# Kernel optimization log

Hardware: AMD Instinct MI355X
Metric: run time of the kernel (lower is better)

Reference implementation:

```python
import jax, jax.numpy as jnp
import numpy as np

WINDOW = 128
LOOK_BACKWARD = 1
LOOK_FORWARD = 0
PAD_VALUE = -1


def look_around(x, backward=LOOK_BACKWARD, forward=LOOK_FORWARD, pad_value=PAD_VALUE):
    # x: [b, windows, window_size, ...]; pad along windows axis, concat along window_size axis
    pad_width = [(0, 0)] * x.ndim
    pad_width[1] = (backward, forward)
    px = jnp.pad(x, pad_width, constant_values=pad_value)
    w = x.shape[1]
    return jnp.concatenate([px[:, i:i + w] for i in range(forward + backward + 1)], axis=2)


def rotate_half(x):
    x1, x2 = jnp.split(x, 2, axis=-1)
    return jnp.concatenate([-x2, x1], axis=-1)


def setup_inputs() -> dict:
    key = jax.random.key(0)
    k1, k2, k3 = jax.random.split(key, 3)
    B, H, N, D = 4, 16, 4096, 64
    return {
        "q": jax.random.normal(k1, (B, H, N, D), dtype=jnp.float32),
        "k": jax.random.normal(k2, (B, H, N, D), dtype=jnp.float32),
        "v": jax.random.normal(k3, (B, H, N, D), dtype=jnp.float32),
    }


def reference(q, k, v):
    B, H, N, D = q.shape
    qf = q.reshape(B * H, N, D)
    kf = k.reshape(B * H, N, D)
    vf = v.reshape(B * H, N, D)

    # --- inline rotary (SinusoidalEmbeddings + apply_rotary_pos_emb) ---
    inv_freq = 1.0 / (10000.0 ** (jnp.arange(0, D, 2, dtype=jnp.float32) / D))  # [D/2]
    t = jnp.arange(N, dtype=jnp.float32)
    half = t[:, None] * inv_freq[None, :]                      # [N, D/2]
    freqs = jnp.concatenate([half, half], axis=-1)             # [N, D]
    cos, sin = jnp.cos(freqs), jnp.sin(freqs)
    qf = qf * cos + rotate_half(qf) * sin
    kf = kf * cos + rotate_half(kf) * sin

    # --- blocked local attention ---
    w = WINDOW
    windows = N // w
    scale = D ** -0.5
    bq = qf.reshape(B * H, windows, w, D)
    bk = look_around(kf.reshape(B * H, windows, w, D))         # [bh, windows, j, D]
    bv = look_around(vf.reshape(B * H, windows, w, D))

    seq = jnp.arange(N).reshape(1, windows, w)
    bq_t = seq[..., :, None]                                   # [1, windows, w, 1]
    bq_k = look_around(seq)[..., None, :]                      # [1, windows, 1, j]

    sim = jnp.einsum('bwie,bwje->bwij', bq, bk) * scale        # [bh, windows, w, j]
    mask_value = -jnp.finfo(sim.dtype).max
    sim = jnp.where(bq_t < bq_k, mask_value, sim)              # causal mask

    attn = jax.nn.softmax(sim, axis=-1)
    out = jnp.einsum('bwij,bwje->bwie', attn, bv)              # [bh, windows, w, D]
    return out.reshape(B, H, N, D)
```

## Files before the change

### kernel.cpp

```cpp
#include <hip/hip_runtime.h>
#include <hip/hip_bf16.h>

typedef __attribute__((ext_vector_type(8))) short  short8;
typedef __attribute__((ext_vector_type(4))) short  short4v;
typedef __attribute__((ext_vector_type(4))) float  float4v;

#define MFMA_QK(A,B,C) __builtin_amdgcn_mfma_f32_16x16x32_bf16(A,B,C,0,0,0)
#define MFMA_PV(A,B,C) __builtin_amdgcn_mfma_f32_16x16x16bf16_1k(A,B,C,0,0,0)

static __device__ __forceinline__ short f2bf(float x) {
  unsigned u = __float_as_uint(x);
  u += 0x7fffu + ((u >> 16) & 1u);
  return (short)(u >> 16);
}

static __device__ __forceinline__ void rope_sc(float rev, float& sn, float& cs) {
  float fr = rev - floorf(rev);
  sn = __builtin_amdgcn_sinf(fr);
  cs = __builtin_amdgcn_cosf(fr);
}

static __device__ __forceinline__ float invfreq_rev(int idx) {
  return exp2f(-0.41524101186092034f * (float)idx) * 0.15915494309189535f;
}

#define N_ 4096
#define D_ 64
#define W_ 128

__global__ __launch_bounds__(256, 2)
void la_fused(const float* __restrict__ qg, const float* __restrict__ kg,
              const float* __restrict__ vg, float* __restrict__ outg)
{
  __shared__ __attribute__((aligned(16))) short Kl[256][72];
  __shared__ __attribute__((aligned(16))) short Vl[64][264];

  const int blk  = blockIdx.x;
  const int w    = blk & 31;
  const int bh   = blk >> 5;
  const int base = bh * (N_ * D_);
  const int tid  = threadIdx.x;

  {
    const float* kb = kg + base;
    const float* vb = vg + base;
#pragma unroll
    for (int it = 0; it < 8; ++it) {
      int tau = it * 256 + tid;
      int j   = tau >> 3;
      int d0  = (tau & 7) << 2;
      int g   = w * W_ - W_ + j;
      float klo[4], khi[4], vlo[4], vhi[4];
      if (g < 0) {
#pragma unroll
        for (int dd = 0; dd < 4; ++dd) { klo[dd]=khi[dd]=vlo[dd]=vhi[dd] = -1.0f; }
      } else {
        float4v a   = *(const float4v*)(kb + g * D_ + d0);
        float4v b   = *(const float4v*)(kb + g * D_ + d0 + 32);
        float4v va  = *(const float4v*)(vb + g * D_ + d0);
        float4v vb2 = *(const float4v*)(vb + g * D_ + d0 + 32);
        const float t = (float)g;
#pragma unroll
        for (int dd = 0; dd < 4; ++dd) {
          float sn, cs; rope_sc(t * invfreq_rev(d0 + dd), sn, cs);
          klo[dd] = a[dd] * cs - b[dd] * sn;
          khi[dd] = b[dd] * cs + a[dd] * sn;
          vlo[dd] = va[dd]; vhi[dd] = vb2[dd];
        }
      }
      short4v k0 = { f2bf(klo[0]), f2bf(klo[1]), f2bf(klo[2]), f2bf(klo[3]) };
      short4v k1 = { f2bf(khi[0]), f2bf(khi[1]), f2bf(khi[2]), f2bf(khi[3]) };
      *(short4v*)&Kl[j][d0]      = k0;
      *(short4v*)&Kl[j][d0 + 32] = k1;
#pragma unroll
      for (int dd = 0; dd < 4; ++dd) {
        Vl[d0 + dd][j]      = f2bf(vlo[dd]);
        Vl[d0 + 32 + dd][j] = f2bf(vhi[dd]);
      }
    }
  }
  __syncthreads();

  const int lane = tid & 63;
  const int wv   = tid >> 6;
  const int il   = lane & 15;
  const int qd   = lane >> 4;

  short8 qf[2][2];
#pragma unroll
  for (int ii = 0; ii < 2; ++ii) {
    const int rw = wv * 32 + ii * 16 + il;
    const int n  = w * W_ + rw;
    const float* qr = qg + base + n * D_ + qd * 8;
    float4v x0 = *(const float4v*)(qr);
    float4v x1 = *(const float4v*)(qr + 4);
    float4v y0 = *(const float4v*)(qr + 32);
    float4v y1 = *(const float4v*)(qr + 36);
    float lo[8], hi[8];
    const float t = (float)n;
#pragma unroll
    for (int jj = 0; jj < 8; ++jj) {
      const int d = qd * 8 + jj;
      float xx = (jj < 4) ? x0[jj & 3] : x1[jj & 3];
      float yy = (jj < 4) ? y0[jj & 3] : y1[jj & 3];
      float sn, cs; rope_sc(t * invfreq_rev(d), sn, cs);
      lo[jj] = xx * cs - yy * sn;
      hi[jj] = yy * cs + xx * sn;
    }
    qf[ii][0] = short8{ f2bf(lo[0]),f2bf(lo[1]),f2bf(lo[2]),f2bf(lo[3]),
                        f2bf(lo[4]),f2bf(lo[5]),f2bf(lo[6]),f2bf(lo[7]) };
    qf[ii][1] = short8{ f2bf(hi[0]),f2bf(hi[1]),f2bf(hi[2]),f2bf(hi[3]),
                        f2bf(hi[4]),f2bf(hi[5]),f2bf(hi[6]),f2bf(hi[7]) };
  }

  float4v S[2][16];
#pragma unroll
  for (int ii = 0; ii < 2; ++ii)
#pragma unroll
    for (int t = 0; t < 16; ++t) { float4v z = {0.f,0.f,0.f,0.f}; S[ii][t] = z; }

#pragma unroll
  for (int t = 0; t < 16; ++t) {
    short8 a0 = *(const short8*)&Kl[t * 16 + il][qd * 8];
    short8 a1 = *(const short8*)&Kl[t * 16 + il][32 + qd * 8];
#pragma unroll
    for (int ii = 0; ii < 2; ++ii) {
      S[ii][t] = MFMA_QK(a0, qf[ii][0], S[ii][t]);
      S[ii][t] = MFMA_QK(a1, qf[ii][1], S[ii][t]);
    }
  }

  short4v P[2][16];
  float   invsum[2];
#pragma unroll
  for (int ii = 0; ii < 2; ++ii) {
    const int rw = wv * 32 + ii * 16 + il;
    float mx = -3.0e38f;
#pragma unroll
    for (int t = 0; t < 16; ++t) {
#pragma unroll
      for (int r = 0; r < 4; ++r) {
        const int j = t * 16 + qd * 4 + r;
        float s = S[ii][t][r] * 0.125f;
        if (j > rw + 128) s = -3.0e38f;
        S[ii][t][r] = s;
        mx = fmaxf(mx, s);
      }
    }
    mx = fmaxf(mx, __shfl_xor(mx, 16));
    mx = fmaxf(mx, __shfl_xor(mx, 32));
    float sum = 0.0f;
#pragma unroll
    for (int t = 0; t < 16; ++t) {
#pragma unroll
      for (int r = 0; r < 4; ++r) {
        float p = __expf(S[ii][t][r] - mx);
        S[ii][t][r] = p;
        sum += p;
      }
    }
    sum += __shfl_xor(sum, 16);
    sum += __shfl_xor(sum, 32);
    invsum[ii] = 1.0f / sum;
#pragma unroll
    for (int t = 0; t < 16; ++t) {
      P[ii][t] = short4v{ f2bf(S[ii][t][0]), f2bf(S[ii][t][1]),
                          f2bf(S[ii][t][2]), f2bf(S[ii][t][3]) };
    }
  }

  float4v O[2][4];
#pragma unroll
  for (int ii = 0; ii < 2; ++ii)
#pragma unroll
    for (int dt = 0; dt < 4; ++dt) { float4v z = {0.f,0.f,0.f,0.f}; O[ii][dt] = z; }

#pragma unroll
  for (int c = 0; c < 16; ++c) {
    short4v af[4];
#pragma unroll
    for (int dt = 0; dt < 4; ++dt)
      af[dt] = *(const short4v*)&Vl[dt * 16 + il][c * 16 + qd * 4];
#pragma unroll
    for (int dt = 0; dt < 4; ++dt) {
      O[0][dt] = MFMA_PV(af[dt], P[0][c], O[0][dt]);
      O[1][dt] = MFMA_PV(af[dt], P[1][c], O[1][dt]);
    }
  }

#pragma unroll
  for (int ii = 0; ii < 2; ++ii) {
    const int n = w * W_ + wv * 32 + ii * 16 + il;
    float* op = outg + base + n * D_;
    const float inv = invsum[ii];
#pragma unroll
    for (int dt = 0; dt < 4; ++dt) {
      float4v o = O[ii][dt];
      o[0] *= inv; o[1] *= inv; o[2] *= inv; o[3] *= inv;
      *(float4v*)(op + dt * 16 + qd * 4) = o;
    }
  }
}

extern "C" void kernel_launch(void* const* d_in, const int* in_sizes, int n_in,
                              void* d_out, int out_size, void* d_ws, size_t ws_size,
                              hipStream_t stream)
{
  const float* q = (const float*)d_in[0];
  const float* k = (const float*)d_in[1];
  const float* v = (const float*)d_in[2];
  float* out = (float*)d_out;
  la_fused<<<dim3(64 * 32), dim3(256), 0, stream>>>(q, k, v, out);
}
```

Baseline: 226.1 us.

## Precompute rotary table, repack V layout, fold scale into Q, cheaper bf16 packing

Adds a small kernel that writes cos/sin tables to the workspace so the main kernel loads rotary factors instead of evaluating sin/cos per element. V is stored in shared memory in a chunked [j/4][d][4] layout with vectorized stores, replacing scalar transposed writes. The softmax scale and log2(e) are folded into Q so softmax uses exp2 and rcp. The mask is only evaluated on tiles that may be masked, and bf16 conversion uses round-half-up with a byte permute. Trade-offs are an extra launch, extra memory traffic for the table reads, and slightly different rounding.

```diff
diff --git a/kernel.cpp b/kernel.cpp
--- a/kernel.cpp
+++ b/kernel.cpp
@@ -1,17 +1,24 @@
 #include <hip/hip_runtime.h>
 #include <hip/hip_bf16.h>
 
-typedef __attribute__((ext_vector_type(8))) short  short8;
-typedef __attribute__((ext_vector_type(4))) short  short4v;
-typedef __attribute__((ext_vector_type(4))) float  float4v;
+typedef __attribute__((ext_vector_type(8))) short    short8;
+typedef __attribute__((ext_vector_type(4))) short    short4v;
+typedef __attribute__((ext_vector_type(4))) float    float4v;
+typedef __attribute__((ext_vector_type(2))) unsigned uint2v;
+typedef __attribute__((ext_vector_type(4))) unsigned uint4v;
 
 #define MFMA_QK(A,B,C) __builtin_amdgcn_mfma_f32_16x16x32_bf16(A,B,C,0,0,0)
 #define MFMA_PV(A,B,C) __builtin_amdgcn_mfma_f32_16x16x16bf16_1k(A,B,C,0,0,0)
 
-static __device__ __forceinline__ short f2bf(float x) {
-  unsigned u = __float_as_uint(x);
-  u += 0x7fffu + ((u >> 16) & 1u);
-  return (short)(u >> 16);
+#define N_ 4096
+#define D_ 64
+#define W_ 128
+#define QSCALE 0.18033688011112042f
+
+static __device__ __forceinline__ unsigned pk2(float a, float b) {
+  unsigned ua = __float_as_uint(a) + 0x8000u;
+  unsigned ub = __float_as_uint(b) + 0x8000u;
+  return __builtin_amdgcn_perm(ub, ua, 0x07060302u);
 }
 
 static __device__ __forceinline__ void rope_sc(float rev, float& sn, float& cs) {
@@ -19,99 +26,148 @@
   sn = __builtin_amdgcn_sinf(fr);
   cs = __builtin_amdgcn_cosf(fr);
 }
-
 static __device__ __forceinline__ float invfreq_rev(int idx) {
   return exp2f(-0.41524101186092034f * (float)idx) * 0.15915494309189535f;
 }
 
-#define N_ 4096
-#define D_ 64
-#define W_ 128
-
+__global__ void gen_tab(float* __restrict__ cosT, float* __restrict__ sinT) {
+  int i = blockIdx.x * 256 + threadIdx.x;
+  int n = i >> 5, d = i & 31;
+  float sn, cs;
+  rope_sc((float)n * invfreq_rev(d), sn, cs);
+  cosT[i] = cs; sinT[i] = sn;
+}
+
+template<bool TAB>
 __global__ __launch_bounds__(256, 2)
 void la_fused(const float* __restrict__ qg, const float* __restrict__ kg,
-              const float* __restrict__ vg, float* __restrict__ outg)
+              const float* __restrict__ vg, float* __restrict__ outg,
+              const float* __restrict__ cosT, const float* __restrict__ sinT)
 {
   __shared__ __attribute__((aligned(16))) short Kl[256][72];
-  __shared__ __attribute__((aligned(16))) short Vl[64][264];
+  __shared__ __attribute__((aligned(16))) short Vt[64][68][4];
 
   const int blk  = blockIdx.x;
   const int w    = blk & 31;
   const int bh   = blk >> 5;
   const int base = bh * (N_ * D_);
   const int tid  = threadIdx.x;
+  const int lane = tid & 63;
+  const int wv   = tid >> 6;
+  const int il   = lane & 15;
+  const int qd   = lane >> 4;
 
   {
     const float* kb = kg + base;
-    const float* vb = vg + base;
 #pragma unroll
     for (int it = 0; it < 8; ++it) {
       int tau = it * 256 + tid;
       int j   = tau >> 3;
       int d0  = (tau & 7) << 2;
       int g   = w * W_ - W_ + j;
-      float klo[4], khi[4], vlo[4], vhi[4];
+      uint2v w0, w1;
       if (g < 0) {
-#pragma unroll
-        for (int dd = 0; dd < 4; ++dd) { klo[dd]=khi[dd]=vlo[dd]=vhi[dd] = -1.0f; }
+        unsigned m1 = pk2(-1.0f, -1.0f);
+        w0 = uint2v{m1, m1}; w1 = w0;
       } else {
-        float4v a   = *(const float4v*)(kb + g * D_ + d0);
-        float4v b   = *(const float4v*)(kb + g * D_ + d0 + 32);
-        float4v va  = *(const float4v*)(vb + g * D_ + d0);
-        float4v vb2 = *(const float4v*)(vb + g * D_ + d0 + 32);
-        const float t = (float)g;
+        float4v a = *(const float4v*)(kb + g * D_ + d0);
+        float4v b = *(const float4v*)(kb + g * D_ + d0 + 32);
+        float4v cs, sn;
+        if constexpr (TAB) {
+          cs = *(const float4v*)(cosT + g * 32 + d0);
+          sn = *(const float4v*)(sinT + g * 32 + d0);
+        } else {
+          const float t = (float)g;
+#pragma unroll
+          for (int dd = 0; dd < 4; ++dd) { float s_, c_; rope_sc(t * invfreq_rev(d0 + dd), s_, c_); sn[dd]=s_; cs[dd]=c_; }
+        }
+        float lo[4], hi[4];
 #pragma unroll
         for (int dd = 0; dd < 4; ++dd) {
-          float sn, cs; rope_sc(t * invfreq_rev(d0 + dd), sn, cs);
-          klo[dd] = a[dd] * cs - b[dd] * sn;
-          khi[dd] = b[dd] * cs + a[dd] * sn;
-          vlo[dd] = va[dd]; vhi[dd] = vb2[dd];
+          lo[dd] = a[dd] * cs[dd] - b[dd] * sn[dd];
+          hi[dd] = b[dd] * cs[dd] + a[dd] * sn[dd];
         }
-      }
-      short4v k0 = { f2bf(klo[0]), f2bf(klo[1]), f2bf(klo[2]), f2bf(klo[3]) };
-      short4v k1 = { f2bf(khi[0]), f2bf(khi[1]), f2bf(khi[2]), f2bf(khi[3]) };
-      *(short4v*)&Kl[j][d0]      = k0;
-      *(short4v*)&Kl[j][d0 + 32] = k1;
+        w0 = uint2v{ pk2(lo[0], lo[1]), pk2(lo[2], lo[3]) };
+        w1 = uint2v{ pk2(hi[0], hi[1]), pk2(hi[2], hi[3]) };
+      }
+      *(uint2v*)&Kl[j][d0]      = w0;
+      *(uint2v*)&Kl[j][d0 + 32] = w1;
+    }
+  }
+
+  {
+    const float* vb = vg + base;
+    const int m  = tid & 15;
+    const int d0 = m << 2;
+#pragma unroll
+    for (int pv = 0; pv < 4; ++pv) {
+      int j0 = ((tid >> 4) + pv * 16) << 2;
+      int g0 = w * W_ - W_ + j0;
+      float vv[4][4];
+      if (g0 < 0) {
+#pragma unroll
+        for (int rr = 0; rr < 4; ++rr)
+#pragma unroll
+          for (int cc = 0; cc < 4; ++cc) vv[rr][cc] = -1.0f;
+      } else {
+#pragma unroll
+        for (int rr = 0; rr < 4; ++rr) {
+          float4v r = *(const float4v*)(vb + (g0 + rr) * D_ + d0);
+          vv[rr][0]=r[0]; vv[rr][1]=r[1]; vv[rr][2]=r[2]; vv[rr][3]=r[3];
+        }
+      }
+      const int chunk = j0 >> 2;
 #pragma unroll
       for (int dd = 0; dd < 4; ++dd) {
-        Vl[d0 + dd][j]      = f2bf(vlo[dd]);
-        Vl[d0 + 32 + dd][j] = f2bf(vhi[dd]);
-      }
-    }
-  }
-  __syncthreads();
-
-  const int lane = tid & 63;
-  const int wv   = tid >> 6;
-  const int il   = lane & 15;
-  const int qd   = lane >> 4;
+        int cc = (dd + m) & 3;
+        uint2v wvv = uint2v{ pk2(vv[0][cc], vv[1][cc]), pk2(vv[2][cc], vv[3][cc]) };
+        *(uint2v*)&Vt[chunk][d0 + cc][0] = wvv;
+      }
+    }
+  }
 
   short8 qf[2][2];
 #pragma unroll
   for (int ii = 0; ii < 2; ++ii) {
-    const int rw = wv * 32 + ii * 16 + il;
-    const int n  = w * W_ + rw;
+    const int n = w * W_ + wv * 32 + ii * 16 + il;
     const float* qr = qg + base + n * D_ + qd * 8;
     float4v x0 = *(const float4v*)(qr);
     float4v x1 = *(const float4v*)(qr + 4);
     float4v y0 = *(const float4v*)(qr + 32);
     float4v y1 = *(const float4v*)(qr + 36);
+    float4v c0, c1, s0, s1;
+    if constexpr (TAB) {
+      c0 = *(const float4v*)(cosT + n * 32 + qd * 8);
+      c1 = *(const float4v*)(cosT + n * 32 + qd * 8 + 4);
+      s0 = *(const float4v*)(sinT + n * 32 + qd * 8);
+      s1 = *(const float4v*)(sinT + n * 32 + qd * 8 + 4);
+    } else {
+      const float t = (float)n;
+#pragma unroll
+      for (int dd = 0; dd < 4; ++dd) {
+        float s_, c_;
+        rope_sc(t * invfreq_rev(qd * 8 + dd), s_, c_);     s0[dd]=s_; c0[dd]=c_;
+        rope_sc(t * invfreq_rev(qd * 8 + 4 + dd), s_, c_); s1[dd]=s_; c1[dd]=c_;
+      }
+    }
     float lo[8], hi[8];
-    const float t = (float)n;
 #pragma unroll
     for (int jj = 0; jj < 8; ++jj) {
-      const int d = qd * 8 + jj;
       float xx = (jj < 4) ? x0[jj & 3] : x1[jj & 3];
       float yy = (jj < 4) ? y0[jj & 3] : y1[jj & 3];
-      float sn, cs; rope_sc(t * invfreq_rev(d), sn, cs);
-      lo[jj] = xx * cs - yy * sn;
-      hi[jj] = yy * cs + xx * sn;
-    }
-    qf[ii][0] = short8{ f2bf(lo[0]),f2bf(lo[1]),f2bf(lo[2]),f2bf(lo[3]),
-                        f2bf(lo[4]),f2bf(lo[5]),f2bf(lo[6]),f2bf(lo[7]) };
-    qf[ii][1] = short8{ f2bf(hi[0]),f2bf(hi[1]),f2bf(hi[2]),f2bf(hi[3]),
-                        f2bf(hi[4]),f2bf(hi[5]),f2bf(hi[6]),f2bf(hi[7]) };
-  }
+      float cs = (jj < 4) ? c0[jj & 3] : c1[jj & 3];
+      float sn = (jj < 4) ? s0[jj & 3] : s1[jj & 3];
+      float xs = xx * QSCALE, ys = yy * QSCALE;
+      lo[jj] = xs * cs - ys * sn;
+      hi[jj] = ys * cs + xs * sn;
+    }
+    uint4v pa = uint4v{ pk2(lo[0],lo[1]), pk2(lo[2],lo[3]), pk2(lo[4],lo[5]), pk2(lo[6],lo[7]) };
+    uint4v pb = uint4v{ pk2(hi[0],hi[1]), pk2(hi[2],hi[3]), pk2(hi[4],hi[5]), pk2(hi[6],hi[7]) };
+    qf[ii][0] = __builtin_bit_cast(short8, pa);
+    qf[ii][1] = __builtin_bit_cast(short8, pb);
+  }
+
+  __syncthreads();
 
   float4v S[2][16];
 #pragma unroll
@@ -134,15 +190,16 @@
   float   invsum[2];
 #pragma unroll
   for (int ii = 0; ii < 2; ++ii) {
-    const int rw = wv * 32 + ii * 16 + il;
-    float mx = -3.0e38f;
+    const int rw   = wv * 32 + ii * 16 + il;
+    const int jcap = rw + 128;
+    float mx = -1.0e30f;
 #pragma unroll
     for (int t = 0; t < 16; ++t) {
+      bool maybe = (t * 16 + 15) > (wv * 32 + ii * 16 + 128);
 #pragma unroll
       for (int r = 0; r < 4; ++r) {
-        const int j = t * 16 + qd * 4 + r;
-        float s = S[ii][t][r] * 0.125f;
-        if (j > rw + 128) s = -3.0e38f;
+        float s = S[ii][t][r];
+        if (maybe) { int j = t * 16 + qd * 4 + r; if (j > jcap) s = -1.0e30f; }
         S[ii][t][r] = s;
         mx = fmaxf(mx, s);
       }
@@ -151,21 +208,20 @@
     mx = fmaxf(mx, __shfl_xor(mx, 32));
     float sum = 0.0f;
 #pragma unroll
-    for (int t = 0; t < 16; ++t) {
+    for (int t = 0; t < 16; ++t)
 #pragma unroll
       for (int r = 0; r < 4; ++r) {
-        float p = __expf(S[ii][t][r] - mx);
+        float p = __builtin_amdgcn_exp2f(S[ii][t][r] - mx);
         S[ii][t][r] = p;
         sum += p;
       }
-    }
     sum += __shfl_xor(sum, 16);
     sum += __shfl_xor(sum, 32);
-    invsum[ii] = 1.0f / sum;
+    invsum[ii] = __builtin_amdgcn_rcpf(sum);
 #pragma unroll
     for (int t = 0; t < 16; ++t) {
-      P[ii][t] = short4v{ f2bf(S[ii][t][0]), f2bf(S[ii][t][1]),
-                          f2bf(S[ii][t][2]), f2bf(S[ii][t][3]) };
+      uint2v pw = uint2v{ pk2(S[ii][t][0], S[ii][t][1]), pk2(S[ii][t][2], S[ii][t][3]) };
+      P[ii][t] = __builtin_bit_cast(short4v, pw);
     }
   }
 
@@ -180,7 +236,7 @@
     short4v af[4];
 #pragma unroll
     for (int dt = 0; dt < 4; ++dt)
-      af[dt] = *(const short4v*)&Vl[dt * 16 + il][c * 16 + qd * 4];
+      af[dt] = *(const short4v*)&Vt[c * 4 + qd][dt * 16 + il][0];
 #pragma unroll
     for (int dt = 0; dt < 4; ++dt) {
       O[0][dt] = MFMA_PV(af[dt], P[0][c], O[0][dt]);
@@ -210,5 +266,13 @@
   const float* k = (const float*)d_in[1];
   const float* v = (const float*)d_in[2];
   float* out = (float*)d_out;
-  la_fused<<<dim3(64 * 32), dim3(256), 0, stream>>>(q, k, v, out);
-}
+  const size_t tabBytes = (size_t)N_ * 32 * 2 * sizeof(float);
+  if (ws_size >= tabBytes) {
+    float* cosT = (float*)d_ws;
+    float* sinT = cosT + N_ * 32;
+    gen_tab<<<dim3(512), dim3(256), 0, stream>>>(cosT, sinT);
+    la_fused<true><<<dim3(64 * 32), dim3(256), 0, stream>>>(q, k, v, out, cosT, sinT);
+  } else {
+    la_fused<false><<<dim3(64 * 32), dim3(256), 0, stream>>>(q, k, v, out, nullptr, nullptr);
+  }
+}
```

Measured after the change: 238.1 us. 5.3% more time.
